# Performance work log

Measured on AMD Instinct MI355X. Metric: run time of the kernel, lower is better.

## Reference

```python
import jax, jax.numpy as jnp
import numpy as np

# --- module hyperparameters (from init_kwargs) ---
NUM_CHANNELS = 31
WINDOW_SIZE = 3
IN_DIM = 2 * WINDOW_SIZE + 1          # 7
GRID_SIZE = 5
SPLINE_ORDER = 3
GRID_RANGE = (-1.0, 1.0)
N_BASIS = GRID_SIZE + SPLINE_ORDER    # 8 spline coefficients per input dim
COEF_LEN = IN_DIM * 1 * N_BASIS       # 56
KAN_PARAMS = COEF_LEN + IN_DIM + IN_DIM  # 70 = coef + univariate_w + residual_w


def bspline_basis(x):
    """Cox-de Boor B-spline bases of order SPLINE_ORDER on a uniform grid.
    x: [...,] -> returns [..., N_BASIS]."""
    lo, hi = GRID_RANGE
    h = (hi - lo) / GRID_SIZE
    # extended knot vector: grid_size + 2*k + 1 knots
    knots = lo + h * jnp.arange(-SPLINE_ORDER, GRID_SIZE + SPLINE_ORDER + 1,
                                dtype=x.dtype)
    xe = x[..., None]
    b = ((xe >= knots[:-1]) & (xe < knots[1:])).astype(x.dtype)
    for p in range(1, SPLINE_ORDER + 1):
        left = (xe - knots[: -(p + 1)]) / (knots[p:-1] - knots[: -(p + 1)]) * b[..., :-1]
        right = (knots[p + 1:] - xe) / (knots[p + 1:] - knots[1:-p]) * b[..., 1:]
        b = left + right
    return b  # [..., N_BASIS]


def setup_inputs() -> dict:
    key = jax.random.key(0)
    k1, k2, k3 = jax.random.split(key, 3)
    B, C, D, H, W = 2, NUM_CHANNELS, IN_DIM, 192, 192
    windowed_x = jax.random.normal(k1, (B, C, D, H, W), dtype=jnp.float32)
    # hypernetwork generator: 3x3 conv  C -> KAN_PARAMS
    gen_w = jax.random.normal(k2, (KAN_PARAMS, C, 3, 3), dtype=jnp.float32) * 0.05
    gen_b = jax.random.normal(k3, (KAN_PARAMS,), dtype=jnp.float32) * 0.05
    return {"windowed_x": windowed_x, "gen_w": gen_w, "gen_b": gen_b}


def reference(windowed_x, gen_w, gen_b):
    B, C, D, H, W = windowed_x.shape
    # shared-params branch: global context -> per-pixel KAN weights
    ctx = windowed_x.mean(axis=2)  # [B, C, H, W]
    wts = jax.lax.conv_general_dilated(
        ctx, gen_w, window_strides=(1, 1), padding="SAME",
        dimension_numbers=("NCHW", "OIHW", "NCHW"))
    wts = wts + gen_b[None, :, None, None]            # [B, P, H, W]
    wts = jnp.moveaxis(wts, 1, -1)                    # [B, H, W, P]
    # unpack per-pixel KAN parameters (out_dim == 1 squeezed)
    coef = wts[..., :COEF_LEN].reshape(B, H, W, D, N_BASIS)   # [B,H,W,7,8]
    uw = wts[..., COEF_LEN:COEF_LEN + D]                      # [B,H,W,7]
    rw = wts[..., COEF_LEN + D:COEF_LEN + 2 * D]              # [B,H,W,7]
    # per-pixel, per-channel spline window evaluation (weights shared over C)
    x = jnp.moveaxis(windowed_x, 2, -1)               # [B, C, H, W, 7]
    basis = bspline_basis(x)                          # [B, C, H, W, 7, 8]
    spline = jnp.einsum("bchwdg,bhwdg,bhwd->bchw", basis, coef, uw)
    resid = jnp.einsum("bchwd,bhwd->bchw", jax.nn.silu(x), rw)
    return spline + resid                             # [B, C, H, W]
```

## Files before the change

kernel.cpp:

```cpp
#include <hip/hip_runtime.h>
#include <math.h>

#define NBATCH 2
#define NC 31
#define ND 7
#define NH 192
#define NW 192
#define HW (NH * NW)
#define NP (NBATCH * HW)
#define NBASIS 8
#define CLEN 56
#define KP 70

#define N4 (NBATCH * NC * (HW / 4))
#define GWB_N (9 * 80 * 32)

#define SMEM_BYTES (KP * 64 * 4)
#define B_WORDS (3 * 66 * 32)

#define KPX 64

typedef __attribute__((ext_vector_type(8))) short s16x8;
typedef __attribute__((ext_vector_type(4))) float f32x4;

__device__ __forceinline__ unsigned short f2bf(float f)
{
    unsigned u = __float_as_uint(f);
    u += 0x7FFFu + ((u >> 16) & 1u);
    return (unsigned short)(u >> 16);
}

__global__ __launch_bounds__(256) void ctx_mean_kernel(
    const float4* __restrict__ x4, float4* __restrict__ ctx4,
    const float* __restrict__ gw, unsigned short* __restrict__ gwb)
{
    const int HW4 = HW / 4;
    int idx = blockIdx.x * 256 + threadIdx.x;
    if (idx < N4) {
        int hw4 = idx % HW4;
        int bc  = idx / HW4;
        const float4* src = x4 + (size_t)bc * (ND * HW4) + hw4;
        float4 a = src[0];
#pragma unroll
        for (int d = 1; d < ND; ++d) {
            float4 v = src[d * HW4];
            a.x += v.x; a.y += v.y; a.z += v.z; a.w += v.w;
        }
        const float inv = 1.0f / 7.0f;
        a.x *= inv; a.y *= inv; a.z *= inv; a.w *= inv;
        ctx4[idx] = a;
        return;
    }
    int e = idx - N4;
    if (e < GWB_N) {
        int s  = e / 2560;
        int r  = e - s * 2560;
        int m  = r >> 5;
        int ic = r & 31;
        float v = (m < KP && ic < NC) ? gw[m * (NC * 9) + ic * 9 + s] : 0.f;
        gwb[e] = f2bf(v);
    }
}

__device__ __forceinline__ float spline_part(float xv, const float* cb, int d)
{
    float t = __builtin_fmaf(xv, 2.5f, 5.5f);
    float fi = floorf(t);
    int i = (int)fi;
    float u = t - fi;
    float u2 = u * u, u3 = u2 * u;
    float um = 1.f - u;
    float w0 = um * um * um * (1.f / 6.f);
    float w3 = u3 * (1.f / 6.f);
    float w1 = (3.f * u3 - 6.f * u2 + 4.f) * (1.f / 6.f);
    float w2 = 1.f - w0 - w1 - w3;
    int j0 = i - 3;
    float sd = 0.f;
#pragma unroll
    for (int k = 0; k < 4; ++k) {
        int j = j0 + k;
        bool valid = ((unsigned)j) < 8u;
        int jc = j & 7;
        float wk = (k == 0) ? w0 : (k == 1) ? w1 : (k == 2) ? w2 : w3;
        float cf = cb[(d * NBASIS + jc) * KPX];
        sd += (valid ? wk : 0.f) * cf;
    }
    return sd;
}

__device__ __forceinline__ float silu(float xv)
{
    return xv / (1.f + __expf(-xv));
}

__global__ __launch_bounds__(256, 8) void fused_kernel(
    const float* __restrict__ ctx, const unsigned short* __restrict__ gwb,
    const float* __restrict__ gb, const float* __restrict__ x,
    float* __restrict__ out)
{
    __shared__ __align__(16) unsigned char smem[SMEM_BYTES];
    unsigned short* Bt = (unsigned short*)smem;
    float* scoef = (float*)smem;

    const int tid  = threadIdx.x;
    const int lane = tid & 63;
    const int wv   = tid >> 6;
    const int gr   = blockIdx.x / 3;
    const int x0   = (blockIdx.x % 3) * 64;
    const int b    = gr / NH;
    const int y    = gr - b * NH;

    if (tid < 3 * 66) {
        int row = tid / 66;
        int col = tid - row * 66;
        int gy = y + row - 1, gx = x0 + col - 1;
        bool ok = (gy >= 0) && (gy < NH) && (gx >= 0) && (gx < NW);
        int cgy = ok ? gy : 0, cgx = ok ? gx : 0;
        const float* src = ctx + (size_t)(b * NC) * HW + cgy * NW + cgx;
        unsigned dw[16];
        if (ok) {
            float v[NC];
#pragma unroll
            for (int ic = 0; ic < NC; ++ic) v[ic] = src[(size_t)ic * HW];
#pragma unroll
            for (int j = 0; j < 16; ++j) {
                unsigned lo = f2bf(v[2 * j]);
                unsigned hi = (2 * j + 1 < NC) ? (unsigned)f2bf(v[2 * j + 1]) : 0u;
                dw[j] = lo | (hi << 16);
            }
        } else {
#pragma unroll
            for (int j = 0; j < 16; ++j) dw[j] = 0u;
        }
        uint4* dst = (uint4*)(Bt + tid * 32);
#pragma unroll
        for (int q = 0; q < 4; ++q)
            dst[q] = make_uint4(dw[4 * q], dw[4 * q + 1], dw[4 * q + 2], dw[4 * q + 3]);
    }

    const int hw = y * NW + x0 + lane;
    const float* xb = x + (size_t)(b * NC) * (ND * HW) + hw;
    const int c0 = wv * 8;
    float cur[2][ND];
    {
        int ca = min(c0, 30), cb2 = min(c0 + 1, 30);
#pragma unroll
        for (int d = 0; d < ND; ++d) {
            cur[0][d] = xb[((size_t)ca * ND + d) * HW];
            cur[1][d] = xb[((size_t)cb2 * ND + d) * HW];
        }
    }
    __syncthreads();

    const int lm = lane & 15;
    const int kb = lane >> 4;

    f32x4 acc[5];
#pragma unroll
    for (int mt = 0; mt < 5; ++mt)
#pragma unroll
        for (int j = 0; j < 4; ++j) {
            int m = mt * 16 + kb * 4 + j;
            acc[mt][j] = (m < KP) ? gb[m] : 0.f;
        }

    const unsigned short* ap = gwb + lm * 32 + kb * 8;
    const unsigned short* bp = Bt + (wv * 16 + lm) * 32 + kb * 8;

#pragma unroll
    for (int s = 0; s < 9; ++s) {
        const int dy = s / 3, dx = s % 3;
        s16x8 bf = *(const s16x8*)(bp + (dy * 66 + dx) * 32);
#pragma unroll
        for (int mt = 0; mt < 5; ++mt) {
            s16x8 af = *(const s16x8*)(ap + (s * 80 + mt * 16) * 32);
            acc[mt] = __builtin_amdgcn_mfma_f32_16x16x32_bf16(af, bf, acc[mt], 0, 0, 0);
        }
    }
    __syncthreads();

    {
        const int px = wv * 16 + lm;
#pragma unroll
        for (int mt = 0; mt < 5; ++mt)
#pragma unroll
            for (int j = 0; j < 4; ++j) {
                int m = mt * 16 + kb * 4 + j;
                if (m < KP) scoef[m * KPX + px] = acc[mt][j];
            }
    }
    __syncthreads();

    const float* cbl = scoef + lane;

    float uw[ND], rw[ND];
#pragma unroll
    for (int d = 0; d < ND; ++d) {
        uw[d] = cbl[(CLEN + d) * KPX];
        rw[d] = cbl[(CLEN + ND + d) * KPX];
    }

    float* ob = out + (b * NC) * HW + hw;

    float nxt[2][ND];
#pragma unroll
    for (int pr = 0; pr < 4; ++pr) {
        int ca = min(c0 + 2 * pr, 30), cb2 = min(c0 + 2 * pr + 1, 30);
        if (pr < 3) {
            int na = min(c0 + 2 * pr + 2, 30), nb = min(c0 + 2 * pr + 3, 30);
#pragma unroll
            for (int d = 0; d < ND; ++d) {
                nxt[0][d] = xb[((size_t)na * ND + d) * HW];
                nxt[1][d] = xb[((size_t)nb * ND + d) * HW];
            }
        }
        float sa = 0.f, sb = 0.f;
#pragma unroll
        for (int d = 0; d < ND; ++d) {
            sa += uw[d] * spline_part(cur[0][d], cbl, d) + rw[d] * silu(cur[0][d]);
            sb += uw[d] * spline_part(cur[1][d], cbl, d) + rw[d] * silu(cur[1][d]);
        }
        ob[(size_t)ca * HW] = sa;
        ob[(size_t)cb2 * HW] = sb;
        if (pr < 3) {
#pragma unroll
            for (int d = 0; d < ND; ++d) {
                cur[0][d] = nxt[0][d];
                cur[1][d] = nxt[1][d];
            }
        }
    }
}

extern "C" void kernel_launch(void* const* d_in, const int* in_sizes, int n_in,
                              void* d_out, int out_size, void* d_ws, size_t ws_size,
                              hipStream_t stream)
{
    const float* x  = (const float*)d_in[0];
    const float* gw = (const float*)d_in[1];
    const float* gb = (const float*)d_in[2];
    float* out = (float*)d_out;

    float* ctx = (float*)d_ws;
    unsigned short* gwb = (unsigned short*)(ctx + (size_t)NBATCH * NC * HW);

    ctx_mean_kernel<<<dim3(N4 / 256 + (GWB_N + 255) / 256), 256, 0, stream>>>(
        (const float4*)x, (float4*)ctx, gw, gwb);
    fused_kernel<<<dim3(NP / 64), 256, 0, stream>>>(ctx, gwb, gb, x, out);
}
```

Measured before the change: 143.2 us.

## Split fused conv+KAN kernel into separate conv and KAN kernels with channel-split grid

Separates the per-pixel MFMA convolution that generates KAN weights from the spline evaluation, writing the 70 weights per pixel to a workspace buffer. The KAN kernel now uses a 2D grid splitting channels across two blocks with four channels per wave, removing clamped duplicate channel work and the serialization of conv and spline phases inside one block. This adds an extra global write and read of the weight tensor and one more kernel launch.

```diff
diff --git a/kernel.cpp b/kernel.cpp
--- a/kernel.cpp
+++ b/kernel.cpp
@@ -15,7 +15,6 @@
 #define N4 (NBATCH * NC * (HW / 4))
 #define GWB_N (9 * 80 * 32)
 
-#define SMEM_BYTES (KP * 64 * 4)
 #define B_WORDS (3 * 66 * 32)
 
 #define KPX 64
@@ -60,6 +59,85 @@
         float v = (m < KP && ic < NC) ? gw[m * (NC * 9) + ic * 9 + s] : 0.f;
         gwb[e] = f2bf(v);
     }
+}
+
+__global__ __launch_bounds__(256) void conv_kernel(
+    const float* __restrict__ ctx, const unsigned short* __restrict__ gwb,
+    const float* __restrict__ gb, float* __restrict__ wts)
+{
+    __shared__ __align__(16) unsigned short Bt[B_WORDS];
+
+    const int tid  = threadIdx.x;
+    const int lane = tid & 63;
+    const int wv   = tid >> 6;
+    const int gr   = blockIdx.x / 3;
+    const int x0   = (blockIdx.x % 3) * 64;
+    const int b    = gr / NH;
+    const int y    = gr - b * NH;
+
+    if (tid < 3 * 66) {
+        int row = tid / 66;
+        int col = tid - row * 66;
+        int gy = y + row - 1, gx = x0 + col - 1;
+        bool ok = (gy >= 0) && (gy < NH) && (gx >= 0) && (gx < NW);
+        int cgy = ok ? gy : 0, cgx = ok ? gx : 0;
+        const float* src = ctx + (size_t)(b * NC) * HW + cgy * NW + cgx;
+        unsigned dw[16];
+        if (ok) {
+            float v[NC];
+#pragma unroll
+            for (int ic = 0; ic < NC; ++ic) v[ic] = src[(size_t)ic * HW];
+#pragma unroll
+            for (int j = 0; j < 16; ++j) {
+                unsigned lo = f2bf(v[2 * j]);
+                unsigned hi = (2 * j + 1 < NC) ? (unsigned)f2bf(v[2 * j + 1]) : 0u;
+                dw[j] = lo | (hi << 16);
+            }
+        } else {
+#pragma unroll
+            for (int j = 0; j < 16; ++j) dw[j] = 0u;
+        }
+        uint4* dst = (uint4*)(Bt + tid * 32);
+#pragma unroll
+        for (int q = 0; q < 4; ++q)
+            dst[q] = make_uint4(dw[4 * q], dw[4 * q + 1], dw[4 * q + 2], dw[4 * q + 3]);
+    }
+    __syncthreads();
+
+    const int lm = lane & 15;
+    const int kb = lane >> 4;
+
+    f32x4 acc[5];
+#pragma unroll
+    for (int mt = 0; mt < 5; ++mt)
+#pragma unroll
+        for (int j = 0; j < 4; ++j) {
+            int m = mt * 16 + kb * 4 + j;
+            acc[mt][j] = (m < KP) ? gb[m] : 0.f;
+        }
+
+    const unsigned short* ap = gwb + lm * 32 + kb * 8;
+    const unsigned short* bp = Bt + (wv * 16 + lm) * 32 + kb * 8;
+
+#pragma unroll
+    for (int s = 0; s < 9; ++s) {
+        const int dy = s / 3, dx = s % 3;
+        s16x8 bf = *(const s16x8*)(bp + (dy * 66 + dx) * 32);
+#pragma unroll
+        for (int mt = 0; mt < 5; ++mt) {
+            s16x8 af = *(const s16x8*)(ap + (s * 80 + mt * 16) * 32);
+            acc[mt] = __builtin_amdgcn_mfma_f32_16x16x32_bf16(af, bf, acc[mt], 0, 0, 0);
+        }
+    }
+
+    const int p = blockIdx.x * 64 + wv * 16 + lm;
+#pragma unroll
+    for (int mt = 0; mt < 5; ++mt)
+#pragma unroll
+        for (int j = 0; j < 4; ++j) {
+            int m = mt * 16 + kb * 4 + j;
+            if (m < KP) wts[(size_t)m * NP + p] = acc[mt][j];
+        }
 }
 
 __device__ __forceinline__ float spline_part(float xv, const float* cb, int d)
@@ -93,105 +171,45 @@
     return xv / (1.f + __expf(-xv));
 }
 
-__global__ __launch_bounds__(256, 8) void fused_kernel(
-    const float* __restrict__ ctx, const unsigned short* __restrict__ gwb,
-    const float* __restrict__ gb, const float* __restrict__ x,
+__global__ __launch_bounds__(256, 4) void kan_kernel(
+    const float* __restrict__ x, const float* __restrict__ wts,
     float* __restrict__ out)
 {
-    __shared__ __align__(16) unsigned char smem[SMEM_BYTES];
-    unsigned short* Bt = (unsigned short*)smem;
-    float* scoef = (float*)smem;
-
+    __shared__ float scoef[KP * KPX];
     const int tid  = threadIdx.x;
     const int lane = tid & 63;
     const int wv   = tid >> 6;
-    const int gr   = blockIdx.x / 3;
-    const int x0   = (blockIdx.x % 3) * 64;
-    const int b    = gr / NH;
-    const int y    = gr - b * NH;
-
-    if (tid < 3 * 66) {
-        int row = tid / 66;
-        int col = tid - row * 66;
-        int gy = y + row - 1, gx = x0 + col - 1;
-        bool ok = (gy >= 0) && (gy < NH) && (gx >= 0) && (gx < NW);
-        int cgy = ok ? gy : 0, cgx = ok ? gx : 0;
-        const float* src = ctx + (size_t)(b * NC) * HW + cgy * NW + cgx;
-        unsigned dw[16];
-        if (ok) {
-            float v[NC];
-#pragma unroll
-            for (int ic = 0; ic < NC; ++ic) v[ic] = src[(size_t)ic * HW];
-#pragma unroll
-            for (int j = 0; j < 16; ++j) {
-                unsigned lo = f2bf(v[2 * j]);
-                unsigned hi = (2 * j + 1 < NC) ? (unsigned)f2bf(v[2 * j + 1]) : 0u;
-                dw[j] = lo | (hi << 16);
-            }
-        } else {
-#pragma unroll
-            for (int j = 0; j < 16; ++j) dw[j] = 0u;
-        }
-        uint4* dst = (uint4*)(Bt + tid * 32);
-#pragma unroll
-        for (int q = 0; q < 4; ++q)
-            dst[q] = make_uint4(dw[4 * q], dw[4 * q + 1], dw[4 * q + 2], dw[4 * q + 3]);
-    }
-
-    const int hw = y * NW + x0 + lane;
+    const int p0   = blockIdx.x * 64;
+    const int b    = p0 / HW;
+    const int hw   = (p0 - b * HW) + lane;
+
+    const int c0 = (blockIdx.y == 0) ? wv * 4
+                                     : ((wv == 3) ? 27 : 16 + wv * 4);
+
     const float* xb = x + (size_t)(b * NC) * (ND * HW) + hw;
-    const int c0 = wv * 8;
     float cur[2][ND];
-    {
-        int ca = min(c0, 30), cb2 = min(c0 + 1, 30);
-#pragma unroll
-        for (int d = 0; d < ND; ++d) {
-            cur[0][d] = xb[((size_t)ca * ND + d) * HW];
-            cur[1][d] = xb[((size_t)cb2 * ND + d) * HW];
-        }
+#pragma unroll
+    for (int d = 0; d < ND; ++d) {
+        cur[0][d] = xb[((size_t)c0 * ND + d) * HW];
+        cur[1][d] = xb[((size_t)(c0 + 1) * ND + d) * HW];
+    }
+
+    for (int f = tid; f < KP * 32; f += 256) {
+        int k = f >> 5;
+        int g = f & 31;
+        float2 v = *(const float2*)(wts + (size_t)k * NP + p0 + g * 2);
+        *(float2*)(scoef + k * KPX + g * 2) = v;
     }
     __syncthreads();
 
-    const int lm = lane & 15;
-    const int kb = lane >> 4;
-
-    f32x4 acc[5];
-#pragma unroll
-    for (int mt = 0; mt < 5; ++mt)
-#pragma unroll
-        for (int j = 0; j < 4; ++j) {
-            int m = mt * 16 + kb * 4 + j;
-            acc[mt][j] = (m < KP) ? gb[m] : 0.f;
-        }
-
-    const unsigned short* ap = gwb + lm * 32 + kb * 8;
-    const unsigned short* bp = Bt + (wv * 16 + lm) * 32 + kb * 8;
-
-#pragma unroll
-    for (int s = 0; s < 9; ++s) {
-        const int dy = s / 3, dx = s % 3;
-        s16x8 bf = *(const s16x8*)(bp + (dy * 66 + dx) * 32);
-#pragma unroll
-        for (int mt = 0; mt < 5; ++mt) {
-            s16x8 af = *(const s16x8*)(ap + (s * 80 + mt * 16) * 32);
-            acc[mt] = __builtin_amdgcn_mfma_f32_16x16x32_bf16(af, bf, acc[mt], 0, 0, 0);
-        }
-    }
-    __syncthreads();
-
-    {
-        const int px = wv * 16 + lm;
-#pragma unroll
-        for (int mt = 0; mt < 5; ++mt)
-#pragma unroll
-            for (int j = 0; j < 4; ++j) {
-                int m = mt * 16 + kb * 4 + j;
-                if (m < KP) scoef[m * KPX + px] = acc[mt][j];
-            }
-    }
-    __syncthreads();
-
     const float* cbl = scoef + lane;
+
+    float nxt[2][ND];
+#pragma unroll
+    for (int d = 0; d < ND; ++d) {
+        nxt[0][d] = xb[((size_t)(c0 + 2) * ND + d) * HW];
+        nxt[1][d] = xb[((size_t)(c0 + 3) * ND + d) * HW];
+    }
 
     float uw[ND], rw[ND];
 #pragma unroll
@@ -202,33 +220,25 @@
 
     float* ob = out + (b * NC) * HW + hw;
 
-    float nxt[2][ND];
-#pragma unroll
-    for (int pr = 0; pr < 4; ++pr) {
-        int ca = min(c0 + 2 * pr, 30), cb2 = min(c0 + 2 * pr + 1, 30);
-        if (pr < 3) {
-            int na = min(c0 + 2 * pr + 2, 30), nb = min(c0 + 2 * pr + 3, 30);
-#pragma unroll
-            for (int d = 0; d < ND; ++d) {
-                nxt[0][d] = xb[((size_t)na * ND + d) * HW];
-                nxt[1][d] = xb[((size_t)nb * ND + d) * HW];
-            }
-        }
+    {
         float sa = 0.f, sb = 0.f;
 #pragma unroll
         for (int d = 0; d < ND; ++d) {
             sa += uw[d] * spline_part(cur[0][d], cbl, d) + rw[d] * silu(cur[0][d]);
             sb += uw[d] * spline_part(cur[1][d], cbl, d) + rw[d] * silu(cur[1][d]);
         }
-        ob[(size_t)ca * HW] = sa;
-        ob[(size_t)cb2 * HW] = sb;
-        if (pr < 3) {
-#pragma unroll
-            for (int d = 0; d < ND; ++d) {
-                cur[0][d] = nxt[0][d];
-                cur[1][d] = nxt[1][d];
-            }
-        }
+        ob[(size_t)c0 * HW] = sa;
+        ob[(size_t)(c0 + 1) * HW] = sb;
+    }
+    {
+        float sa = 0.f, sb = 0.f;
+#pragma unroll
+        for (int d = 0; d < ND; ++d) {
+            sa += uw[d] * spline_part(nxt[0][d], cbl, d) + rw[d] * silu(nxt[0][d]);
+            sb += uw[d] * spline_part(nxt[1][d], cbl, d) + rw[d] * silu(nxt[1][d]);
+        }
+        ob[(size_t)(c0 + 2) * HW] = sa;
+        ob[(size_t)(c0 + 3) * HW] = sb;
     }
 }
 
@@ -243,8 +253,10 @@
 
     float* ctx = (float*)d_ws;
     unsigned short* gwb = (unsigned short*)(ctx + (size_t)NBATCH * NC * HW);
+    float* wts = (float*)(gwb + GWB_N);
 
     ctx_mean_kernel<<<dim3(N4 / 256 + (GWB_N + 255) / 256), 256, 0, stream>>>(
         (const float4*)x, (float4*)ctx, gw, gwb);
-    fused_kernel<<<dim3(NP / 64), 256, 0, stream>>>(ctx, gwb, gb, x, out);
-}
+    conv_kernel<<<dim3(NP / 64), 256, 0, stream>>>(ctx, gwb, gb, wts);
+    kan_kernel<<<dim3(NP / 64, 2), 256, 0, stream>>>(x, wts, out);
+}
```

Result: slower. 146.2 us (+2.1%).
